# Kernel tuning notes

Measured on AMD Instinct MI355X. Metric: run time of the kernel, lower is better.

The kernel has to match this reference:

```python
import jax, jax.numpy as jnp
import numpy as np

jax.config.update("jax_enable_x64", True)  # torch casts to double for matrix_exp

EPS_DIAG = 1e-6


def setup_inputs() -> dict:
    key = jax.random.key(0)
    B, D, NB, S = 32, 128, 8, 128
    ks = jax.random.split(key, 9)
    return {
        "z0r": jax.random.normal(ks[0], (B, D), jnp.float32),
        "z0i": jax.random.normal(ks[1], (B, D), jnp.float32),
        # uniform grid: dt = time_steps[0] = 0.01, diffs == dt (uniform branch)
        "time_steps": (jnp.arange(S, dtype=jnp.float32) + 1.0) * 0.01,
        "k_coeffs": jax.random.normal(ks[2], (B, NB), jnp.float32),
        "r_coeffs": jax.random.normal(ks[3], (B, NB), jnp.float32),
        "alpha": jax.random.normal(ks[4], (B, 1), jnp.float32),
        "beta": jax.random.normal(ks[5], (B, 1), jnp.float32),
        "K_bases": jax.random.normal(ks[6], (NB, D, D), jnp.float32) * 0.01,
        "R_bases": jax.random.normal(ks[7], (NB, D, D), jnp.float32) * 0.01,
    }


def _build_generator(k_coeffs, r_coeffs, alpha, beta, K_bases, R_bases):
    # A = alpha * skew(K_sum) + beta * -(R_sum^T @ R_sum), per batch element
    K_sum = jnp.einsum("bn,nij->bij", k_coeffs, K_bases)
    R_sum = jnp.einsum("bn,nij->bij", r_coeffs, R_bases)
    skew = K_sum - jnp.swapaxes(K_sum, -1, -2)
    neg_gram = -jnp.einsum("bji,bjk->bik", R_sum, R_sum)  # -(R^T @ R)
    return alpha[..., None] * skew + beta[..., None] * neg_gram  # (B, D, D)


def _propagators(A, time_steps, uniform):
    D = A.shape[-1]
    S = time_steps.shape[0]
    if uniform:
        dt = time_steps[0]
        A64 = A.astype(jnp.float64) * dt.astype(jnp.float64) + EPS_DIAG * jnp.eye(D, dtype=jnp.float64)
        M = jax.vmap(jax.scipy.linalg.expm)(A64).astype(jnp.complex64)  # (B, D, D)
        # cumulative matrix powers M, M^2, ..., M^S via O(log S) associative scan
        Ms = jnp.broadcast_to(M[:, None], (M.shape[0], S, D, D))
        props = jax.lax.associative_scan(jnp.matmul, Ms, axis=1)
    else:
        A_t = A[:, None].astype(jnp.float64) * time_steps.astype(jnp.float64)[None, :, None, None]
        props = jax.vmap(jax.vmap(jax.scipy.linalg.expm))(A_t).astype(jnp.complex64)
    return props  # (B, S, D, D)


def reference(z0r, z0i, time_steps, k_coeffs, r_coeffs, alpha, beta, K_bases, R_bases):
    ts = np.asarray(time_steps)
    uniform = ts.shape[0] <= 1 or np.allclose(ts[1:] - ts[:-1], ts[0], atol=1e-6)
    A = _build_generator(k_coeffs, r_coeffs, alpha, beta, K_bases, R_bases)
    props = _propagators(A, time_steps, uniform)
    z = (z0r + 1j * z0i).astype(jnp.complex64)  # (B, D)
    # z_evolved[b, s, o] = sum_i z[b, i] * props[b, s, o, i]
    return jnp.einsum("bi,bsoi->bso", z, props)
```

## Files before the change

### kernel.cpp

```cpp
#include <hip/hip_runtime.h>

#define BATCH   32
#define DIM     128
#define NBASES  8
#define SSTEPS  128
#define LDA     136

typedef __attribute__((ext_vector_type(8))) short s8v;
typedef __attribute__((ext_vector_type(4))) short s4v;
typedef __attribute__((ext_vector_type(4))) float f4v;

__device__ __forceinline__ f4v mf(s8v a, s8v b, f4v c) {
    return __builtin_amdgcn_mfma_f32_16x16x32_bf16(a, b, c, 0, 0, 0);
}
__device__ __forceinline__ s8v ld8(const short* p) {
    return *reinterpret_cast<const s8v*>(p);
}
__device__ __forceinline__ void st4(short* p, s4v v) {
    *reinterpret_cast<s4v*>(p) = v;
}
__device__ __forceinline__ float upbf(short h) {
    return __uint_as_float(((unsigned)(unsigned short)h) << 16);
}
__device__ __forceinline__ void splitbf(float v, short& hi, short& lo) {
    const unsigned u = __float_as_uint(v);
    hi = (short)(u >> 16);
    const float fh = __uint_as_float(u & 0xffff0000u);
    lo = (short)(__float_as_uint(v - fh) >> 16);
}

__device__ __forceinline__ void write_out(float* __restrict__ outF, int b, int sidx,
                                          int o, int c, float val,
                                          int interleaved, int out_size)
{
    if (interleaved) {
        const int oi = ((b * SSTEPS + sidx) * DIM + o) * 2 + c;
        if (oi < out_size) outF[oi] = val;
    } else if (c == 0) {
        const int oi = (b * SSTEPS + sidx) * DIM + o;
        if (oi < out_size) outF[oi] = val;
    }
}

__device__ __forceinline__ void mm_full(const short* __restrict__ Ah,
                                        const short* __restrict__ Al,
                                        const short* __restrict__ Bh,
                                        const short* __restrict__ Bl,
                                        f4v acc[2][2], int mb, int nb, int lane)
{
    const int l15 = lane & 15, quad = lane >> 4;
    #pragma unroll
    for (int kk = 0; kk < DIM; kk += 32) {
        const int ko = kk + quad * 8;
        const s8v a0h = ld8(Ah + (mb +      l15) * LDA + ko);
        const s8v a0l = ld8(Al + (mb +      l15) * LDA + ko);
        const s8v a1h = ld8(Ah + (mb + 16 + l15) * LDA + ko);
        const s8v a1l = ld8(Al + (mb + 16 + l15) * LDA + ko);
        #pragma unroll
        for (int ni = 0; ni < 2; ++ni) {
            const s8v bh = ld8(Bh + (nb + ni * 16 + l15) * LDA + ko);
            const s8v bl = ld8(Bl + (nb + ni * 16 + l15) * LDA + ko);
            acc[0][ni] = mf(a0h, bh, acc[0][ni]);
            acc[0][ni] = mf(a0h, bl, acc[0][ni]);
            acc[0][ni] = mf(a0l, bh, acc[0][ni]);
            acc[1][ni] = mf(a1h, bh, acc[1][ni]);
            acc[1][ni] = mf(a1h, bl, acc[1][ni]);
            acc[1][ni] = mf(a1l, bh, acc[1][ni]);
        }
    }
}

__global__ __launch_bounds__(1024, 1)
void htg_mfma(const float* __restrict__ z0r, const float* __restrict__ z0i,
              const float* __restrict__ ts,  const float* __restrict__ kco,
              const float* __restrict__ rco, const float* __restrict__ alp,
              const float* __restrict__ bet, const float* __restrict__ KB,
              const float* __restrict__ RB,  float* __restrict__ outF,
              int interleaved, int out_size)
{
    __shared__ short nm_hi[DIM * LDA], nm_lo[DIM * LDA];
    __shared__ short tr_hi[DIM * LDA], tr_lo[DIM * LDA];
    __shared__ short ht_hi[32 * LDA],  ht_lo[32 * LDA];
    __shared__ float s_part[1024];

    const int b = blockIdx.x, t = threadIdx.x;
    const int w = t >> 6, lane = t & 63;
    const int l15 = lane & 15, quad = lane >> 4;
    const f4v z4 = {0.f, 0.f, 0.f, 0.f};
    const int mb = (w & 3) * 32, nb = (w >> 2) * 32;

    {
        float rc[NBASES], kc[NBASES];
        #pragma unroll
        for (int n = 0; n < NBASES; ++n) {
            rc[n] = rco[b * NBASES + n];
            kc[n] = kco[b * NBASES + n];
        }
        #pragma unroll
        for (int q = 0; q < 4; ++q) {
            const int e = q * 4096 + t * 4;
            float4 r4 = {0.f, 0.f, 0.f, 0.f}, k4 = {0.f, 0.f, 0.f, 0.f};
            #pragma unroll
            for (int n = 0; n < NBASES; ++n) {
                const float4 rv = *reinterpret_cast<const float4*>(RB + n * DIM * DIM + e);
                const float4 kv = *reinterpret_cast<const float4*>(KB + n * DIM * DIM + e);
                r4.x += rc[n] * rv.x; r4.y += rc[n] * rv.y;
                r4.z += rc[n] * rv.z; r4.w += rc[n] * rv.w;
                k4.x += kc[n] * kv.x; k4.y += kc[n] * kv.y;
                k4.z += kc[n] * kv.z; k4.w += kc[n] * kv.w;
            }
            const int r = e >> 7, c = e & 127;
            const float rr[4] = {r4.x, r4.y, r4.z, r4.w};
            const float kk[4] = {k4.x, k4.y, k4.z, k4.w};
            s4v kh, kl;
            #pragma unroll
            for (int j = 0; j < 4; ++j) {
                short hi, lo;
                splitbf(rr[j], hi, lo);
                tr_hi[(c + j) * LDA + r] = hi; tr_lo[(c + j) * LDA + r] = lo;
                splitbf(kk[j], hi, lo);
                kh[j] = hi; kl[j] = lo;
            }
            st4(&nm_hi[r * LDA + c], kh);
            st4(&nm_lo[r * LDA + c], kl);
        }
        if (t < 2 * DIM) {
            const int c = t >> 7, o = t & 127;
            const float zv = (c == 0) ? z0r[b * DIM + o] : z0i[b * DIM + o];
            short hi, lo; splitbf(zv, hi, lo);
            ht_hi[c * LDA + o] = hi; ht_lo[c * LDA + o] = lo;
        }
    }
    __syncthreads();

    f4v acc[2][2];

    #pragma unroll
    for (int i = 0; i < 2; ++i)
        #pragma unroll
        for (int j = 0; j < 2; ++j) acc[i][j] = z4;
    mm_full(tr_hi, tr_lo, tr_hi, tr_lo, acc, mb, nb, lane);
    __syncthreads();
    {
        const float alpha = alp[b], beta = bet[b], dtf = ts[0];
        #pragma unroll
        for (int mi = 0; mi < 2; ++mi)
            #pragma unroll
            for (int ni = 0; ni < 2; ++ni)
                #pragma unroll
                for (int r = 0; r < 4; ++r) {
                    const int row = mb + mi * 16 + quad * 4 + r;
                    const int col = nb + ni * 16 + l15;
                    const float k1 = upbf(nm_hi[row * LDA + col]) + upbf(nm_lo[row * LDA + col]);
                    const float k2 = upbf(nm_hi[col * LDA + row]) + upbf(nm_lo[col * LDA + row]);
                    float x = (alpha * (k1 - k2) - beta * acc[mi][ni][r]) * dtf;
                    if (row == col) x += 1e-6f;
                    acc[mi][ni][r] = x;
                }
    }
    __syncthreads();
    #pragma unroll
    for (int mi = 0; mi < 2; ++mi)
        #pragma unroll
        for (int ni = 0; ni < 2; ++ni) {
            const int row0 = mb + mi * 16 + quad * 4;
            const int col  = nb + ni * 16 + l15;
            s4v h4, l4;
            #pragma unroll
            for (int r = 0; r < 4; ++r) {
                short hi, lo;
                splitbf(acc[mi][ni][r], hi, lo);
                nm_hi[(row0 + r) * LDA + col] = hi;
                nm_lo[(row0 + r) * LDA + col] = lo;
                h4[r] = hi; l4[r] = lo;
            }
            st4(&tr_hi[col * LDA + row0], h4);
            st4(&tr_lo[col * LDA + row0], l4);
        }
    __syncthreads();

    float a1v[2][2][4];
    #pragma unroll
    for (int i = 0; i < 2; ++i)
        #pragma unroll
        for (int j = 0; j < 2; ++j) acc[i][j] = z4;
    mm_full(nm_hi, nm_lo, tr_hi, tr_lo, acc, mb, nb, lane);
    __syncthreads();
    #pragma unroll
    for (int mi = 0; mi < 2; ++mi)
        #pragma unroll
        for (int ni = 0; ni < 2; ++ni) {
            const int row0 = mb + mi * 16 + quad * 4;
            const int col  = nb + ni * 16 + l15;
            s4v h4, l4;
            #pragma unroll
            for (int r = 0; r < 4; ++r) {
                const int row = row0 + r;
                const float xv = upbf(nm_hi[row * LDA + col]) + upbf(nm_lo[row * LDA + col]);
                const float cv = acc[mi][ni][r];
                a1v[mi][ni][r] = ((row == col) ? 1.f : 0.f) + xv + 0.5f * cv;
                const float a2 = xv * (1.f / 6.f) + cv * (1.f / 24.f);
                short hi, lo;
                splitbf(cv, hi, lo);
                nm_hi[row * LDA + col] = hi;
                nm_lo[row * LDA + col] = lo;
                splitbf(a2, hi, lo);
                h4[r] = hi; l4[r] = lo;
            }
            st4(&tr_hi[col * LDA + row0], h4);
            st4(&tr_lo[col * LDA + row0], l4);
        }
    __syncthreads();

    #pragma unroll
    for (int mi = 0; mi < 2; ++mi)
        #pragma unroll
        for (int ni = 0; ni < 2; ++ni)
            #pragma unroll
            for (int r = 0; r < 4; ++r) acc[mi][ni][r] = a1v[mi][ni][r];
    mm_full(nm_hi, nm_lo, tr_hi, tr_lo, acc, mb, nb, lane);
    __syncthreads();
    #pragma unroll
    for (int mi = 0; mi < 2; ++mi)
        #pragma unroll
        for (int ni = 0; ni < 2; ++ni) {
            const int row0 = mb + mi * 16 + quad * 4;
            const int col  = nb + ni * 16 + l15;
            s4v h4, l4;
            #pragma unroll
            for (int r = 0; r < 4; ++r) {
                short hi, lo;
                splitbf(acc[mi][ni][r], hi, lo);
                nm_hi[(row0 + r) * LDA + col] = hi;
                nm_lo[(row0 + r) * LDA + col] = lo;
                h4[r] = hi; l4[r] = lo;
            }
            st4(&tr_hi[col * LDA + row0], h4);
            st4(&tr_lo[col * LDA + row0], l4);
        }
    __syncthreads();

    #pragma unroll
    for (int stage = 0; stage < 4; ++stage) {
        const int J = 1 << stage;
        f4v ar = z4;
        #pragma unroll
        for (int i = 0; i < 2; ++i)
            #pragma unroll
            for (int j = 0; j < 2; ++j) acc[i][j] = z4;
        if (w < 8) {
            #pragma unroll
            for (int kk = 0; kk < DIM; kk += 32) {
                const int ko = kk + quad * 8;
                const s8v rah = ld8(nm_hi + (w * 16 + l15) * LDA + ko);
                const s8v ral = ld8(nm_lo + (w * 16 + l15) * LDA + ko);
                const s8v rbh = ld8(ht_hi + l15 * LDA + ko);
                const s8v rbl = ld8(ht_lo + l15 * LDA + ko);
                ar = mf(rah, rbh, ar);
                ar = mf(rah, rbl, ar);
                ar = mf(ral, rbh, ar);
            }
        }
        mm_full(nm_hi, nm_lo, tr_hi, tr_lo, acc, mb, nb, lane);
        __syncthreads();
        if (w < 8 && l15 < 2 * J) {
            const int o0 = w * 16 + quad * 4;
            const int sidx = (l15 >> 1) + J - 1;
            s4v h4, l4;
            #pragma unroll
            for (int r = 0; r < 4; ++r) {
                short hi, lo;
                splitbf(ar[r], hi, lo);
                h4[r] = hi; l4[r] = lo;
                write_out(outF, b, sidx, o0 + r, l15 & 1, ar[r], interleaved, out_size);
            }
            st4(&ht_hi[(l15 + 2 * J) * LDA + o0], h4);
            st4(&ht_lo[(l15 + 2 * J) * LDA + o0], l4);
        }
        #pragma unroll
        for (int mi = 0; mi < 2; ++mi)
            #pragma unroll
            for (int ni = 0; ni < 2; ++ni) {
                const int row0 = mb + mi * 16 + quad * 4;
                const int col  = nb + ni * 16 + l15;
                s4v h4, l4;
                #pragma unroll
                for (int r = 0; r < 4; ++r) {
                    short hi, lo;
                    splitbf(acc[mi][ni][r], hi, lo);
                    nm_hi[(row0 + r) * LDA + col] = hi;
                    nm_lo[(row0 + r) * LDA + col] = lo;
                    h4[r] = hi; l4[r] = lo;
                }
                st4(&tr_hi[col * LDA + row0], h4);
                st4(&tr_lo[col * LDA + row0], l4);
            }
        __syncthreads();
    }

    const int sw = w >> 1, ct = w & 1;
    s8v vah[4], val[4];
    #pragma unroll
    for (int k4 = 0; k4 < 4; ++k4) {
        const int ko = k4 * 32 + quad * 8;
        vah[k4] = ld8(nm_hi + (sw * 16 + l15) * LDA + ko);
        val[k4] = ld8(nm_lo + (sw * 16 + l15) * LDA + ko);
    }
    for (int q = 1; q <= 7; ++q) {
        f4v a2 = z4;
        #pragma unroll
        for (int k4 = 0; k4 < 4; ++k4) {
            const int ko = k4 * 32 + quad * 8;
            const s8v bh = ld8(ht_hi + (ct * 16 + l15) * LDA + ko);
            const s8v bl = ld8(ht_lo + (ct * 16 + l15) * LDA + ko);
            a2 = mf(vah[k4], bh, a2);
            a2 = mf(vah[k4], bl, a2);
            a2 = mf(val[k4], bh, a2);
        }
        __syncthreads();
        {
            const int o0 = sw * 16 + quad * 4;
            const int n = ct * 16 + l15;
            const int sidx = 16 * q + (n >> 1) - 1;
            s4v h4, l4;
            #pragma unroll
            for (int r = 0; r < 4; ++r) {
                short hi, lo;
                splitbf(a2[r], hi, lo);
                h4[r] = hi; l4[r] = lo;
                write_out(outF, b, sidx, o0 + r, n & 1, a2[r], interleaved, out_size);
            }
            if (q < 7 || n < 2) {
                st4(&ht_hi[n * LDA + o0], h4);
                st4(&ht_lo[n * LDA + o0], l4);
            }
        }
        __syncthreads();
    }

    {
        const int o = t & 127, c = (t >> 7) & 1, kq = t >> 8;
        const int k0 = kq * 32;
        float a = 0.f;
        #pragma unroll 8
        for (int i = k0; i < k0 + 32; ++i)
            a += (upbf(tr_hi[i * LDA + o]) + upbf(tr_lo[i * LDA + o]))
               * (upbf(ht_hi[c * LDA + i]) + upbf(ht_lo[c * LDA + i]));
        s_part[t] = a;
    }
    __syncthreads();
    if (t < 2 * DIM) {
        const int o = t & 127, c = t >> 7;
        const float a = s_part[t] + s_part[t + 256] + s_part[t + 512] + s_part[t + 768];
        write_out(outF, b, 127, o, c, a, interleaved, out_size);
    }
}

extern "C" void kernel_launch(void* const* d_in, const int* in_sizes, int n_in,
                              void* d_out, int out_size, void* d_ws, size_t ws_size,
                              hipStream_t stream)
{
    (void)in_sizes; (void)n_in; (void)d_ws; (void)ws_size;
    const float* z0r = (const float*)d_in[0];
    const float* z0i = (const float*)d_in[1];
    const float* ts  = (const float*)d_in[2];
    const float* kco = (const float*)d_in[3];
    const float* rco = (const float*)d_in[4];
    const float* alp = (const float*)d_in[5];
    const float* bet = (const float*)d_in[6];
    const float* KB  = (const float*)d_in[7];
    const float* RB  = (const float*)d_in[8];
    float* outF = (float*)d_out;

    const int interleaved = (out_size >= 2 * BATCH * SSTEPS * DIM) ? 1 : 0;

    htg_mfma<<<dim3(BATCH), dim3(1024), 0, stream>>>(
        z0r, z0i, ts, kco, rco, alp, bet, KB, RB, outF, interleaved, out_size);
}
```

Measured before the change: 121.7 us.

## Compute transposed product tiles via dual MFMA to avoid scalar LDS scatter stores

mm_full gains a DUAL mode that also accumulates the transposed output tile (B^T A^T) with extra MFMAs. Each wave can then write both the row-major and column-major copies with vectorized 4-element LDS stores instead of scattered scalar stores. The change also keeps X in registers instead of re-reading it from LDS, vectorizes the K transpose read, aliases s_part onto nm_hi, and sets waves_per_eu. It doubles MFMA work in the squaring stages in exchange for fewer LDS bank-conflicted stores, and it adds register pressure.

```diff
diff --git a/kernel.cpp b/kernel.cpp
--- a/kernel.cpp
+++ b/kernel.cpp
@@ -15,6 +15,9 @@
 }
 __device__ __forceinline__ s8v ld8(const short* p) {
     return *reinterpret_cast<const s8v*>(p);
+}
+__device__ __forceinline__ s4v ld4(const short* p) {
+    return *reinterpret_cast<const s4v*>(p);
 }
 __device__ __forceinline__ void st4(short* p, s4v v) {
     *reinterpret_cast<s4v*>(p) = v;
@@ -42,35 +45,43 @@
     }
 }
 
+template<bool DUAL>
 __device__ __forceinline__ void mm_full(const short* __restrict__ Ah,
                                         const short* __restrict__ Al,
                                         const short* __restrict__ Bh,
                                         const short* __restrict__ Bl,
-                                        f4v acc[2][2], int mb, int nb, int lane)
+                                        f4v acc[2][2], f4v acct[2][2],
+                                        int mb, int nb, int lane)
 {
     const int l15 = lane & 15, quad = lane >> 4;
     #pragma unroll
     for (int kk = 0; kk < DIM; kk += 32) {
         const int ko = kk + quad * 8;
-        const s8v a0h = ld8(Ah + (mb +      l15) * LDA + ko);
-        const s8v a0l = ld8(Al + (mb +      l15) * LDA + ko);
-        const s8v a1h = ld8(Ah + (mb + 16 + l15) * LDA + ko);
-        const s8v a1l = ld8(Al + (mb + 16 + l15) * LDA + ko);
-        #pragma unroll
-        for (int ni = 0; ni < 2; ++ni) {
-            const s8v bh = ld8(Bh + (nb + ni * 16 + l15) * LDA + ko);
-            const s8v bl = ld8(Bl + (nb + ni * 16 + l15) * LDA + ko);
-            acc[0][ni] = mf(a0h, bh, acc[0][ni]);
-            acc[0][ni] = mf(a0h, bl, acc[0][ni]);
-            acc[0][ni] = mf(a0l, bh, acc[0][ni]);
-            acc[1][ni] = mf(a1h, bh, acc[1][ni]);
-            acc[1][ni] = mf(a1h, bl, acc[1][ni]);
-            acc[1][ni] = mf(a1l, bh, acc[1][ni]);
-        }
-    }
-}
-
-__global__ __launch_bounds__(1024, 1)
+        s8v ah[2], al[2], bh[2], bl[2];
+        #pragma unroll
+        for (int i = 0; i < 2; ++i) {
+            ah[i] = ld8(Ah + (mb + i * 16 + l15) * LDA + ko);
+            al[i] = ld8(Al + (mb + i * 16 + l15) * LDA + ko);
+            bh[i] = ld8(Bh + (nb + i * 16 + l15) * LDA + ko);
+            bl[i] = ld8(Bl + (nb + i * 16 + l15) * LDA + ko);
+        }
+        #pragma unroll
+        for (int mi = 0; mi < 2; ++mi)
+            #pragma unroll
+            for (int ni = 0; ni < 2; ++ni) {
+                acc[mi][ni] = mf(ah[mi], bh[ni], acc[mi][ni]);
+                acc[mi][ni] = mf(ah[mi], bl[ni], acc[mi][ni]);
+                acc[mi][ni] = mf(al[mi], bh[ni], acc[mi][ni]);
+                if (DUAL) {
+                    acct[ni][mi] = mf(bh[ni], ah[mi], acct[ni][mi]);
+                    acct[ni][mi] = mf(bl[ni], ah[mi], acct[ni][mi]);
+                    acct[ni][mi] = mf(bh[ni], al[mi], acct[ni][mi]);
+                }
+            }
+    }
+}
+
+__global__ __launch_bounds__(1024) __attribute__((amdgpu_waves_per_eu(4, 4)))
 void htg_mfma(const float* __restrict__ z0r, const float* __restrict__ z0i,
               const float* __restrict__ ts,  const float* __restrict__ kco,
               const float* __restrict__ rco, const float* __restrict__ alp,
@@ -81,7 +92,7 @@
     __shared__ short nm_hi[DIM * LDA], nm_lo[DIM * LDA];
     __shared__ short tr_hi[DIM * LDA], tr_lo[DIM * LDA];
     __shared__ short ht_hi[32 * LDA],  ht_lo[32 * LDA];
-    __shared__ float s_part[1024];
+    float* s_part = reinterpret_cast<float*>(nm_hi);
 
     const int b = blockIdx.x, t = threadIdx.x;
     const int w = t >> 6, lane = t & 63;
@@ -133,30 +144,36 @@
     }
     __syncthreads();
 
-    f4v acc[2][2];
+    f4v acc[2][2], acct[2][2];
+    float xsave[2][2][4];
 
     #pragma unroll
     for (int i = 0; i < 2; ++i)
         #pragma unroll
         for (int j = 0; j < 2; ++j) acc[i][j] = z4;
-    mm_full(tr_hi, tr_lo, tr_hi, tr_lo, acc, mb, nb, lane);
+    mm_full<false>(tr_hi, tr_lo, tr_hi, tr_lo, acc, acct, mb, nb, lane);
     __syncthreads();
     {
         const float alpha = alp[b], beta = bet[b], dtf = ts[0];
         #pragma unroll
         for (int mi = 0; mi < 2; ++mi)
             #pragma unroll
-            for (int ni = 0; ni < 2; ++ni)
+            for (int ni = 0; ni < 2; ++ni) {
+                const int row0 = mb + mi * 16 + quad * 4;
+                const int col  = nb + ni * 16 + l15;
+                const s4v k2h = ld4(&nm_hi[col * LDA + row0]);
+                const s4v k2l = ld4(&nm_lo[col * LDA + row0]);
                 #pragma unroll
                 for (int r = 0; r < 4; ++r) {
-                    const int row = mb + mi * 16 + quad * 4 + r;
-                    const int col = nb + ni * 16 + l15;
+                    const int row = row0 + r;
                     const float k1 = upbf(nm_hi[row * LDA + col]) + upbf(nm_lo[row * LDA + col]);
-                    const float k2 = upbf(nm_hi[col * LDA + row]) + upbf(nm_lo[col * LDA + row]);
+                    const float k2 = upbf(k2h[r]) + upbf(k2l[r]);
                     float x = (alpha * (k1 - k2) - beta * acc[mi][ni][r]) * dtf;
                     if (row == col) x += 1e-6f;
                     acc[mi][ni][r] = x;
+                    xsave[mi][ni][r] = x;
                 }
+            }
     }
     __syncthreads();
     #pragma unroll
@@ -179,12 +196,11 @@
         }
     __syncthreads();
 
-    float a1v[2][2][4];
     #pragma unroll
     for (int i = 0; i < 2; ++i)
         #pragma unroll
-        for (int j = 0; j < 2; ++j) acc[i][j] = z4;
-    mm_full(nm_hi, nm_lo, tr_hi, tr_lo, acc, mb, nb, lane);
+        for (int j = 0; j < 2; ++j) { acc[i][j] = z4; acct[i][j] = z4; }
+    mm_full<true>(nm_hi, nm_lo, tr_hi, tr_lo, acc, acct, mb, nb, lane);
     __syncthreads();
     #pragma unroll
     for (int mi = 0; mi < 2; ++mi)
@@ -196,20 +212,33 @@
             #pragma unroll
             for (int r = 0; r < 4; ++r) {
                 const int row = row0 + r;
-                const float xv = upbf(nm_hi[row * LDA + col]) + upbf(nm_lo[row * LDA + col]);
+                const float xv = xsave[mi][ni][r];
                 const float cv = acc[mi][ni][r];
-                a1v[mi][ni][r] = ((row == col) ? 1.f : 0.f) + xv + 0.5f * cv;
                 const float a2 = xv * (1.f / 6.f) + cv * (1.f / 24.f);
-                short hi, lo;
-                splitbf(cv, hi, lo);
-                nm_hi[row * LDA + col] = hi;
-                nm_lo[row * LDA + col] = lo;
+                xsave[mi][ni][r] = ((row == col) ? 1.f : 0.f) + xv + 0.5f * cv;
+                short hi, lo;
                 splitbf(a2, hi, lo);
                 h4[r] = hi; l4[r] = lo;
             }
             st4(&tr_hi[col * LDA + row0], h4);
             st4(&tr_lo[col * LDA + row0], l4);
         }
+    #pragma unroll
+    for (int ti = 0; ti < 2; ++ti)
+        #pragma unroll
+        for (int tj = 0; tj < 2; ++tj) {
+            const int rt0 = nb + ti * 16 + quad * 4;
+            const int ct  = mb + tj * 16 + l15;
+            s4v h4, l4;
+            #pragma unroll
+            for (int r = 0; r < 4; ++r) {
+                short hi, lo;
+                splitbf(acct[ti][tj][r], hi, lo);
+                h4[r] = hi; l4[r] = lo;
+            }
+            st4(&nm_hi[ct * LDA + rt0], h4);
+            st4(&nm_lo[ct * LDA + rt0], l4);
+        }
     __syncthreads();
 
     #pragma unroll
@@ -217,8 +246,8 @@
         #pragma unroll
         for (int ni = 0; ni < 2; ++ni)
             #pragma unroll
-            for (int r = 0; r < 4; ++r) acc[mi][ni][r] = a1v[mi][ni][r];
-    mm_full(nm_hi, nm_lo, tr_hi, tr_lo, acc, mb, nb, lane);
+            for (int r = 0; r < 4; ++r) acc[mi][ni][r] = xsave[mi][ni][r];
+    mm_full<false>(nm_hi, nm_lo, tr_hi, tr_lo, acc, acct, mb, nb, lane);
     __syncthreads();
     #pragma unroll
     for (int mi = 0; mi < 2; ++mi)
@@ -247,7 +276,7 @@
         #pragma unroll
         for (int i = 0; i < 2; ++i)
             #pragma unroll
-            for (int j = 0; j < 2; ++j) acc[i][j] = z4;
+            for (int j = 0; j < 2; ++j) { acc[i][j] = z4; acct[i][j] = z4; }
         if (w < 8) {
             #pragma unroll
             for (int kk = 0; kk < DIM; kk += 32) {
@@ -261,7 +290,7 @@
                 ar = mf(ral, rbh, ar);
             }
         }
-        mm_full(nm_hi, nm_lo, tr_hi, tr_lo, acc, mb, nb, lane);
+        mm_full<true>(nm_hi, nm_lo, tr_hi, tr_lo, acc, acct, mb, nb, lane);
         __syncthreads();
         if (w < 8 && l15 < 2 * J) {
             const int o0 = w * 16 + quad * 4;
@@ -288,12 +317,26 @@
                 for (int r = 0; r < 4; ++r) {
                     short hi, lo;
                     splitbf(acc[mi][ni][r], hi, lo);
-                    nm_hi[(row0 + r) * LDA + col] = hi;
-                    nm_lo[(row0 + r) * LDA + col] = lo;
                     h4[r] = hi; l4[r] = lo;
                 }
                 st4(&tr_hi[col * LDA + row0], h4);
                 st4(&tr_lo[col * LDA + row0], l4);
+            }
+        #pragma unroll
+        for (int ti = 0; ti < 2; ++ti)
+            #pragma unroll
+            for (int tj = 0; tj < 2; ++tj) {
+                const int rt0 = nb + ti * 16 + quad * 4;
+                const int ct  = mb + tj * 16 + l15;
+                s4v h4, l4;
+                #pragma unroll
+                for (int r = 0; r < 4; ++r) {
+                    short hi, lo;
+                    splitbf(acct[ti][tj][r], hi, lo);
+                    h4[r] = hi; l4[r] = lo;
+                }
+                st4(&nm_hi[ct * LDA + rt0], h4);
+                st4(&nm_lo[ct * LDA + rt0], l4);
             }
         __syncthreads();
     }
```

After: 122.6 us. No clear change (+0.7%).
